# Kernel optimization log

Measured on AMD Instinct MI355X. Metric: run time of the kernel, lower is better.

Reference implementation:

```python
import jax, jax.numpy as jnp
import numpy as np

DIM = 1024


def setup_inputs() -> dict:
    key = jax.random.key(0)
    kx, kq, kk, kv, kp = jax.random.split(key, 5)
    scale = 1.0 / np.sqrt(DIM)  # ~PyTorch Linear init scale
    return {
        "x": jax.random.normal(kx, (4, 4096, DIM), dtype=jnp.float32),
        "Wq": jax.random.normal(kq, (DIM, DIM), dtype=jnp.float32) * scale,
        "Wk": jax.random.normal(kk, (DIM, DIM), dtype=jnp.float32) * scale,
        "Wv": jax.random.normal(kv, (DIM, DIM), dtype=jnp.float32) * scale,
        "Wp": jax.random.normal(kp, (DIM, DIM), dtype=jnp.float32) * scale,
    }


def reference(x, Wq, Wk, Wv, Wp):
    # nn.Linear: y = x @ W^T (no bias)
    q = jnp.einsum("bsd,ed->bse", x, Wq)
    k = jnp.einsum("bsd,ed->bse", x, Wk)
    v = jnp.einsum("bsd,ed->bse", x, Wv)
    dim = x.shape[-1]
    # maxP 'readout' scaling: 1/dim (instead of 1/sqrt(dim))
    scores = jnp.einsum("bqd,bkd->bqk", q, k) / dim
    attn = jax.nn.softmax(scores, axis=-1)
    out = jnp.einsum("bqk,bkd->bqd", attn, v)
    return jnp.einsum("bsd,ed->bse", out, Wp)
```

## Files before the change

### kernel.cpp

```cpp
#include <hip/hip_runtime.h>

typedef unsigned short u16;
typedef __attribute__((ext_vector_type(8))) short bf16x8;
typedef __attribute__((ext_vector_type(4))) float f32x4;
typedef __attribute__((ext_vector_type(4))) unsigned short us4;
typedef __attribute__((ext_vector_type(8))) unsigned short us8;

__device__ __forceinline__ u16 f2us(float f) {
  union { float f; unsigned u; } a; a.f = f;
  unsigned u = a.u;
  u += 0x7fffu + ((u >> 16) & 1u);
  return (u16)(u >> 16);
}
__device__ __forceinline__ float us2f(u16 h) {
  union { unsigned u; float f; } a; a.u = ((unsigned)h) << 16;
  return a.f;
}

#define GLDS(g, l) __builtin_amdgcn_global_load_lds( \
    (const __attribute__((address_space(1))) void*)(g), \
    (__attribute__((address_space(3))) void*)(l), 16, 0, 0)

__global__ __launch_bounds__(256) void convert_all(
    const float* __restrict__ x, const float* __restrict__ Wq,
    const float* __restrict__ Wk, const float* __restrict__ Wv,
    const float* __restrict__ Wp, u16* __restrict__ xb, u16* __restrict__ wb) {
  const int bid = blockIdx.x;
  const float* src;
  u16* dst;
  int off;
  if (bid < 16384) {
    src = x; dst = xb; off = bid * 256 + threadIdx.x;
  } else {
    const int w = (bid - 16384) >> 10;
    const int lb = (bid - 16384) & 1023;
    src = (w == 0) ? Wq : (w == 1) ? Wk : (w == 2) ? Wv : Wp;
    dst = wb + (size_t)w * 1048576;
    off = lb * 256 + threadIdx.x;
  }
  f32x4 v = ((const f32x4*)src)[off];
  us4 o;
  o.x = f2us(v.x); o.y = f2us(v.y); o.z = f2us(v.z); o.w = f2us(v.w);
  ((us4*)dst)[off] = o;
}

#define MFMA_QUAD(QR, QC)                                                        \
  do {                                                                           \
    __builtin_amdgcn_s_setprio(1);                                               \
    _Pragma("unroll") for (int m = 0; m < 4; ++m)                                \
    _Pragma("unroll") for (int n = 0; n < 2; ++n)                                \
    _Pragma("unroll") for (int s = 0; s < 2; ++s)                                \
      acc[(QR)*4 + m][(QC)*2 + n] = __builtin_amdgcn_mfma_f32_16x16x32_bf16(     \
          af[(QR)*4 + m][s], bf[(QC)*2 + n][s], acc[(QR)*4 + m][(QC)*2 + n],     \
          0, 0, 0);                                                              \
    __builtin_amdgcn_s_setprio(0);                                               \
  } while (0)

#define STAGE_A(buf, h, kb)                                                  \
  do {                                                                       \
    const int su_ = (h) * 128 * lda + (kb);                                  \
    GLDS(Ap + aoff0 + su_, As + (buf) * 16384 + (h) * 8192 + ldst0);         \
    GLDS(Ap + aoff1 + su_, As + (buf) * 16384 + (h) * 8192 + ldst1);         \
  } while (0)

#define STAGE_B(buf, h, kb)                                                  \
  do {                                                                       \
    const int su_ = (h) * 128 * ldb + (kb);                                  \
    GLDS(Bp + boff0 + su_, Bs + (buf) * 16384 + (h) * 8192 + ldst0);         \
    GLDS(Bp + boff1 + su_, Bs + (buf) * 16384 + (h) * 8192 + ldst1);         \
  } while (0)

template <int EP>
__global__ __launch_bounds__(512, 2) void gemm256(
    const u16* __restrict__ A0, const u16* __restrict__ A1,
    const u16* __restrict__ A2, const u16* __restrict__ A3,
    const u16* __restrict__ B0, const u16* __restrict__ B1,
    const u16* __restrict__ B2, const u16* __restrict__ B3,
    void* C0, void* C1, void* C2, void* C3,
    int K, int lda, int ldb, int ldc, float scale) {
  __shared__ u16 As[32768];
  __shared__ u16 Bs[32768];
  const int tid = threadIdx.x;
  const int lane = tid & 63;
  const int wid = tid >> 6;
  const int wm = wid >> 2;
  const int wn = wid & 3;
  const int z = blockIdx.z;
  const u16* A = (z == 0) ? A0 : (z == 1) ? A1 : (z == 2) ? A2 : A3;
  const u16* B = (z == 0) ? B0 : (z == 1) ? B1 : (z == 2) ? B2 : B3;
  void* C = (z == 0) ? C0 : (z == 1) ? C1 : (z == 2) ? C2 : C3;

  const int gx = gridDim.x;
  const int nwg = gx * (int)gridDim.y;
  const int orig = (int)blockIdx.y * gx + (int)blockIdx.x;
  const int swz = (orig & 7) * (nwg >> 3) + (orig >> 3);
  const long trow = (long)(swz / gx) * 256;
  const long tcol = (long)(swz % gx) * 256;

  const int srow = tid >> 3;
  const int sgrp = (tid & 7) ^ (srow & 7);
  const int aoff0 = srow * lda + sgrp * 8;
  const int aoff1 = aoff0 + (lda << 6);
  const int boff0 = srow * ldb + sgrp * 8;
  const int boff1 = boff0 + (ldb << 6);
  const int ldst0 = (tid & ~63) * 8;
  const int ldst1 = ldst0 + 4096;
  const u16* Ap = A + trow * lda;
  const u16* Bp = B + tcol * ldb;

  const int l15x64 = (lane & 15) * 64;
  const int cs0 = ((((lane >> 4) * 8)) ^ ((lane & 7) * 8)) + l15x64;
  const int cs1 = ((32 + ((lane >> 4) * 8)) ^ ((lane & 7) * 8)) + l15x64;

  f32x4 acc[8][4];
  f32x4 zero = {0.f, 0.f, 0.f, 0.f};
#pragma unroll
  for (int m = 0; m < 8; ++m)
#pragma unroll
    for (int n = 0; n < 4; ++n) acc[m][n] = zero;

  const int NT = K >> 6;
  const int kmask = K - 1;

  STAGE_A(0, 0, 0);
  STAGE_A(0, 1, 0);
  STAGE_B(0, 0, 0);
  STAGE_B(0, 1, 0);
  STAGE_A(1, 0, 64 & kmask);
  STAGE_A(1, 1, 64 & kmask);
  asm volatile("s_waitcnt vmcnt(4)" ::: "memory");
  __builtin_amdgcn_s_barrier();

  for (int t = 0; t < NT; ++t) {
    const int cur = t & 1, nxt = cur ^ 1;
    const int kb1 = ((t + 1) << 6) & kmask;
    const int kb2 = ((t + 2) << 6) & kmask;
    const u16* Acur = As + cur * 16384 + wm * 8192;
    const u16* Bcur = Bs + cur * 16384 + (wn >> 1) * 8192 + (wn & 1) * 4096;
    bf16x8 af[8][2], bf[4][2];

#pragma unroll
    for (int m = 0; m < 4; ++m) {
      af[m][0] = *(const bf16x8*)(Acur + m * 1024 + cs0);
      af[m][1] = *(const bf16x8*)(Acur + m * 1024 + cs1);
    }
#pragma unroll
    for (int n = 0; n < 2; ++n) {
      bf[n][0] = *(const bf16x8*)(Bcur + n * 1024 + cs0);
      bf[n][1] = *(const bf16x8*)(Bcur + n * 1024 + cs1);
    }
    STAGE_B(nxt, 0, kb1);
    __builtin_amdgcn_s_barrier();
    MFMA_QUAD(0, 0);

#pragma unroll
    for (int m = 0; m < 4; ++m) {
      af[4 + m][0] = *(const bf16x8*)(Acur + (4 + m) * 1024 + cs0);
      af[4 + m][1] = *(const bf16x8*)(Acur + (4 + m) * 1024 + cs1);
    }
    STAGE_B(nxt, 1, kb1);
    __builtin_amdgcn_s_barrier();
    MFMA_QUAD(1, 0);

#pragma unroll
    for (int n = 0; n < 2; ++n) {
      bf[2 + n][0] = *(const bf16x8*)(Bcur + (2 + n) * 1024 + cs0);
      bf[2 + n][1] = *(const bf16x8*)(Bcur + (2 + n) * 1024 + cs1);
    }
    __builtin_amdgcn_s_barrier();
    MFMA_QUAD(0, 1);

    STAGE_A(cur, 0, kb2);
    STAGE_A(cur, 1, kb2);
    __builtin_amdgcn_s_barrier();
    MFMA_QUAD(1, 1);
    asm volatile("s_waitcnt vmcnt(4)" ::: "memory");
  }

  asm volatile("s_waitcnt vmcnt(0)" ::: "memory");

  if (EP == 0 || (EP == 3 && z != 2)) {
    u16* Cb = (u16*)C;
#pragma unroll
    for (int m = 0; m < 8; ++m) {
      int gr = (int)trow + wm * 128 + m * 16 + ((lane >> 4) << 2);
#pragma unroll
      for (int n = 0; n < 4; ++n) {
        int gc = (int)tcol + wn * 64 + n * 16 + (lane & 15);
        f32x4 v = acc[m][n];
#pragma unroll
        for (int j = 0; j < 4; ++j) Cb[(size_t)(gr + j) * ldc + gc] = f2us(v[j] * scale);
      }
    }
  } else if (EP == 3) {
    u16* Ct = (u16*)C;
#pragma unroll
    for (int m = 0; m < 8; ++m) {
      int gr = (int)trow + wm * 128 + m * 16 + ((lane >> 4) << 2);
      int b = gr >> 12;
      int sl = gr & 4095;
      u16* base = Ct + ((size_t)b << 22) + sl;
#pragma unroll
      for (int n = 0; n < 4; ++n) {
        int gc = (int)tcol + wn * 64 + n * 16 + (lane & 15);
        f32x4 v = acc[m][n];
        us4 o;
        o.x = f2us(v[0] * scale); o.y = f2us(v[1] * scale);
        o.z = f2us(v[2] * scale); o.w = f2us(v[3] * scale);
        *(us4*)(base + (size_t)gc * 4096) = o;
      }
    }
  } else {
    float* Cf = (float*)C;
#pragma unroll
    for (int m = 0; m < 8; ++m) {
      int gr = (int)trow + wm * 128 + m * 16 + ((lane >> 4) << 2);
#pragma unroll
      for (int n = 0; n < 4; ++n) {
        int gc = (int)tcol + wn * 64 + n * 16 + (lane & 15);
        f32x4 v = acc[m][n];
#pragma unroll
        for (int j = 0; j < 4; ++j) Cf[(size_t)(gr + j) * ldc + gc] = v[j] * scale;
      }
    }
  }
}

__global__ __launch_bounds__(256) void softmax_all(u16* S0, u16* S1, u16* S2, u16* S3) {
  const int row = blockIdx.x;
  const int b = row >> 12;
  u16* S = (b == 0) ? S0 : (b == 1) ? S1 : (b == 2) ? S2 : S3;
  const int t = threadIdx.x;
  const int lane = t & 63;
  const int wave = t >> 6;
  u16* p = S + (size_t)(row & 4095) * 4096 + t * 16;
  us8 r0 = *(const us8*)p;
  us8 r1 = *(const us8*)(p + 8);
  float f[16];
#pragma unroll
  for (int j = 0; j < 8; ++j) { f[j] = us2f(r0[j]); f[8 + j] = us2f(r1[j]); }

  float mx = f[0];
#pragma unroll
  for (int j = 1; j < 16; ++j) mx = fmaxf(mx, f[j]);
#pragma unroll
  for (int o = 32; o > 0; o >>= 1) mx = fmaxf(mx, __shfl_xor(mx, o));
  __shared__ float rmax[4], rsum[4];
  if (lane == 0) rmax[wave] = mx;
  __syncthreads();
  mx = fmaxf(fmaxf(rmax[0], rmax[1]), fmaxf(rmax[2], rmax[3]));

  float e[16], s = 0.f;
#pragma unroll
  for (int j = 0; j < 16; ++j) { e[j] = __expf(f[j] - mx); s += e[j]; }
#pragma unroll
  for (int o = 32; o > 0; o >>= 1) s += __shfl_xor(s, o);
  if (lane == 0) rsum[wave] = s;
  __syncthreads();
  s = rsum[0] + rsum[1] + rsum[2] + rsum[3];
  float inv = 1.f / s;

  us8 o0, o1;
#pragma unroll
  for (int j = 0; j < 8; ++j) { o0[j] = f2us(e[j] * inv); o1[j] = f2us(e[8 + j] * inv); }
  *(us8*)p = o0;
  *(us8*)(p + 8) = o1;
}

extern "C" void kernel_launch(void* const* d_in, const int* in_sizes, int n_in,
                              void* d_out, int out_size, void* d_ws, size_t ws_size,
                              hipStream_t stream) {
  (void)in_sizes; (void)n_in; (void)out_size;
  const float* x  = (const float*)d_in[0];
  const float* Wq = (const float*)d_in[1];
  const float* Wk = (const float*)d_in[2];
  const float* Wv = (const float*)d_in[3];
  const float* Wp = (const float*)d_in[4];

  if (ws_size < 209715200) return;
  char* ws = (char*)d_ws;
  u16* xb  = (u16*)(ws);
  u16* wqb = (u16*)(ws + 33554432);
  u16* wkb = wqb + 1048576;
  u16* wvb = wkb + 1048576;
  u16* wpb = wvb + 1048576;
  u16* Qb  = (u16*)(ws + 41943040);
  u16* Kb  = (u16*)(ws + 75497472);
  u16* Vt  = (u16*)(ws + 109051904);
  u16* Ssp = (u16*)(ws + 142606336);
  u16* O   = (u16*)(ws + 176160768);

  u16* S0 = (u16*)d_out;
  u16* S1 = S0 + 16777216;
  u16* S2 = xb;
  u16* S3 = Ssp;

  convert_all<<<20480, 256, 0, stream>>>(x, Wq, Wk, Wv, Wp, xb, wqb);

  gemm256<3><<<dim3(4, 64, 3), 512, 0, stream>>>(
      xb, xb, xb, xb, wqb, wkb, wvb, wvb, Qb, Kb, Vt, Vt,
      1024, 1024, 1024, 1024, 1.f);

  const u16 *Q0 = Qb, *Q1 = Qb + 4194304, *Q2 = Qb + 8388608, *Q3 = Qb + 12582912;
  const u16 *K0 = Kb, *K1 = Kb + 4194304, *K2 = Kb + 8388608, *K3 = Kb + 12582912;
  gemm256<0><<<dim3(16, 16, 4), 512, 0, stream>>>(Q0, Q1, Q2, Q3, K0, K1, K2, K3,
                                                  S0, S1, S2, S3, 1024, 1024, 1024, 4096,
                                                  1.f / 1024.f);

  softmax_all<<<16384, 256, 0, stream>>>(S0, S1, S2, S3);

  const u16 *V0 = Vt, *V1 = Vt + 4194304, *V2 = Vt + 8388608, *V3 = Vt + 12582912;
  u16 *O0 = O, *O1 = O + 4194304, *O2 = O + 8388608, *O3 = O + 12582912;
  gemm256<0><<<dim3(4, 16, 4), 512, 0, stream>>>(S0, S1, S2, S3, V0, V1, V2, V3,
                                                 O0, O1, O2, O3, 4096, 4096, 4096, 1024, 1.f);

  gemm256<2><<<dim3(4, 64, 1), 512, 0, stream>>>(O, O, O, O, wpb, wpb, wpb, wpb,
                                                 d_out, d_out, d_out, d_out,
                                                 1024, 1024, 1024, 1024, 1.f);
}
```

Baseline: 438.0 us.

## Switch GEMM inner loop from 16x16x32 to 32x32x16 bf16 MFMA tiles

Replaces the 16x16x32 MFMA fragments with 32x32x16 MFMA instructions. This changes the per-wave accumulator layout to 4x2 tiles of 32x32, the LDS fragment addressing (swizzled offsets over 32 rows and four k-slices), and all three epilogues so they match the new output lane mapping. Larger MFMA tiles cut the number of LDS fragment reads and MFMA issues per FLOP. The costs are longer-latency instructions, different register pressure, and epilogue stores that are less contiguous in some paths.

```diff
diff --git a/kernel.cpp b/kernel.cpp
--- a/kernel.cpp
+++ b/kernel.cpp
@@ -3,6 +3,7 @@
 typedef unsigned short u16;
 typedef __attribute__((ext_vector_type(8))) short bf16x8;
 typedef __attribute__((ext_vector_type(4))) float f32x4;
+typedef __attribute__((ext_vector_type(16))) float f32x16;
 typedef __attribute__((ext_vector_type(4))) unsigned short us4;
 typedef __attribute__((ext_vector_type(8))) unsigned short us8;
 
@@ -44,15 +45,15 @@
   ((us4*)dst)[off] = o;
 }
 
-#define MFMA_QUAD(QR, QC)                                                        \
+#define MFMA_PAIR(MA, MB, NT)                                                    \
   do {                                                                           \
     __builtin_amdgcn_s_setprio(1);                                               \
-    _Pragma("unroll") for (int m = 0; m < 4; ++m)                                \
-    _Pragma("unroll") for (int n = 0; n < 2; ++n)                                \
-    _Pragma("unroll") for (int s = 0; s < 2; ++s)                                \
-      acc[(QR)*4 + m][(QC)*2 + n] = __builtin_amdgcn_mfma_f32_16x16x32_bf16(     \
-          af[(QR)*4 + m][s], bf[(QC)*2 + n][s], acc[(QR)*4 + m][(QC)*2 + n],     \
-          0, 0, 0);                                                              \
+    _Pragma("unroll") for (int ks = 0; ks < 4; ++ks) {                           \
+      acc[MA][NT] = __builtin_amdgcn_mfma_f32_32x32x16_bf16(                     \
+          af[MA][ks], bf[NT][ks], acc[MA][NT], 0, 0, 0);                         \
+      acc[MB][NT] = __builtin_amdgcn_mfma_f32_32x32x16_bf16(                     \
+          af[MB][ks], bf[NT][ks], acc[MB][NT], 0, 0, 0);                         \
+    }                                                                            \
     __builtin_amdgcn_s_setprio(0);                                               \
   } while (0)
 
@@ -108,16 +109,19 @@
   const u16* Ap = A + trow * lda;
   const u16* Bp = B + tcol * ldb;
 
-  const int l15x64 = (lane & 15) * 64;
-  const int cs0 = ((((lane >> 4) * 8)) ^ ((lane & 7) * 8)) + l15x64;
-  const int cs1 = ((32 + ((lane >> 4) * 8)) ^ ((lane & 7) * 8)) + l15x64;
-
-  f32x4 acc[8][4];
-  f32x4 zero = {0.f, 0.f, 0.f, 0.f};
-#pragma unroll
-  for (int m = 0; m < 8; ++m)
-#pragma unroll
-    for (int n = 0; n < 4; ++n) acc[m][n] = zero;
+  const int l31x64 = (lane & 31) * 64;
+  const int cb = (lane >> 5) * 8;
+  const int xr = (lane & 7) * 8;
+  const int cs_[4] = {((0 + cb) ^ xr) + l31x64, ((16 + cb) ^ xr) + l31x64,
+                      ((32 + cb) ^ xr) + l31x64, ((48 + cb) ^ xr) + l31x64};
+
+  f32x16 acc[4][2];
+#pragma unroll
+  for (int mt = 0; mt < 4; ++mt)
+#pragma unroll
+    for (int nt = 0; nt < 2; ++nt)
+#pragma unroll
+      for (int j = 0; j < 16; ++j) acc[mt][nt][j] = 0.f;
 
   const int NT = K >> 6;
   const int kmask = K - 1;
@@ -137,43 +141,37 @@
     const int kb2 = ((t + 2) << 6) & kmask;
     const u16* Acur = As + cur * 16384 + wm * 8192;
     const u16* Bcur = Bs + cur * 16384 + (wn >> 1) * 8192 + (wn & 1) * 4096;
-    bf16x8 af[8][2], bf[4][2];
-
-#pragma unroll
-    for (int m = 0; m < 4; ++m) {
-      af[m][0] = *(const bf16x8*)(Acur + m * 1024 + cs0);
-      af[m][1] = *(const bf16x8*)(Acur + m * 1024 + cs1);
-    }
-#pragma unroll
-    for (int n = 0; n < 2; ++n) {
-      bf[n][0] = *(const bf16x8*)(Bcur + n * 1024 + cs0);
-      bf[n][1] = *(const bf16x8*)(Bcur + n * 1024 + cs1);
+    bf16x8 af[4][4], bf[2][4];
+
+#pragma unroll
+    for (int ks = 0; ks < 4; ++ks) {
+      af[0][ks] = *(const bf16x8*)(Acur + 0 * 2048 + cs_[ks]);
+      af[1][ks] = *(const bf16x8*)(Acur + 1 * 2048 + cs_[ks]);
+      bf[0][ks] = *(const bf16x8*)(Bcur + 0 * 2048 + cs_[ks]);
     }
     STAGE_B(nxt, 0, kb1);
     __builtin_amdgcn_s_barrier();
-    MFMA_QUAD(0, 0);
-
-#pragma unroll
-    for (int m = 0; m < 4; ++m) {
-      af[4 + m][0] = *(const bf16x8*)(Acur + (4 + m) * 1024 + cs0);
-      af[4 + m][1] = *(const bf16x8*)(Acur + (4 + m) * 1024 + cs1);
+    MFMA_PAIR(0, 1, 0);
+
+#pragma unroll
+    for (int ks = 0; ks < 4; ++ks) {
+      af[2][ks] = *(const bf16x8*)(Acur + 2 * 2048 + cs_[ks]);
+      af[3][ks] = *(const bf16x8*)(Acur + 3 * 2048 + cs_[ks]);
     }
     STAGE_B(nxt, 1, kb1);
     __builtin_amdgcn_s_barrier();
-    MFMA_QUAD(1, 0);
-
-#pragma unroll
-    for (int n = 0; n < 2; ++n) {
-      bf[2 + n][0] = *(const bf16x8*)(Bcur + (2 + n) * 1024 + cs0);
-      bf[2 + n][1] = *(const bf16x8*)(Bcur + (2 + n) * 1024 + cs1);
-    }
+    MFMA_PAIR(2, 3, 0);
+
+#pragma unroll
+    for (int ks = 0; ks < 4; ++ks)
+      bf[1][ks] = *(const bf16x8*)(Bcur + 1 * 2048 + cs_[ks]);
     __builtin_amdgcn_s_barrier();
-    MFMA_QUAD(0, 1);
+    MFMA_PAIR(0, 1, 1);
 
     STAGE_A(cur, 0, kb2);
     STAGE_A(cur, 1, kb2);
     __builtin_amdgcn_s_barrier();
-    MFMA_QUAD(1, 1);
+    MFMA_PAIR(2, 3, 1);
     asm volatile("s_waitcnt vmcnt(4)" ::: "memory");
   }
 
@@ -182,47 +180,53 @@
   if (EP == 0 || (EP == 3 && z != 2)) {
     u16* Cb = (u16*)C;
 #pragma unroll
-    for (int m = 0; m < 8; ++m) {
-      int gr = (int)trow + wm * 128 + m * 16 + ((lane >> 4) << 2);
-#pragma unroll
-      for (int n = 0; n < 4; ++n) {
-        int gc = (int)tcol + wn * 64 + n * 16 + (lane & 15);
-        f32x4 v = acc[m][n];
-#pragma unroll
-        for (int j = 0; j < 4; ++j) Cb[(size_t)(gr + j) * ldc + gc] = f2us(v[j] * scale);
+    for (int mt = 0; mt < 4; ++mt)
+#pragma unroll
+      for (int nt = 0; nt < 2; ++nt) {
+        const int gc = (int)tcol + wn * 64 + nt * 32 + (lane & 31);
+        const int gr0 = (int)trow + wm * 128 + mt * 32 + ((lane >> 5) << 2);
+        f32x16 v = acc[mt][nt];
+#pragma unroll
+        for (int j = 0; j < 16; ++j) {
+          const int row = gr0 + (j & 3) + ((j >> 2) << 3);
+          Cb[(size_t)row * ldc + gc] = f2us(v[j] * scale);
+        }
       }
-    }
   } else if (EP == 3) {
     u16* Ct = (u16*)C;
 #pragma unroll
-    for (int m = 0; m < 8; ++m) {
-      int gr = (int)trow + wm * 128 + m * 16 + ((lane >> 4) << 2);
-      int b = gr >> 12;
-      int sl = gr & 4095;
-      u16* base = Ct + ((size_t)b << 22) + sl;
-#pragma unroll
-      for (int n = 0; n < 4; ++n) {
-        int gc = (int)tcol + wn * 64 + n * 16 + (lane & 15);
-        f32x4 v = acc[m][n];
-        us4 o;
-        o.x = f2us(v[0] * scale); o.y = f2us(v[1] * scale);
-        o.z = f2us(v[2] * scale); o.w = f2us(v[3] * scale);
-        *(us4*)(base + (size_t)gc * 4096) = o;
+    for (int mt = 0; mt < 4; ++mt)
+#pragma unroll
+      for (int nt = 0; nt < 2; ++nt) {
+        const int gc = (int)tcol + wn * 64 + nt * 32 + (lane & 31);
+        const int gr0 = (int)trow + wm * 128 + mt * 32 + ((lane >> 5) << 2);
+        f32x16 v = acc[mt][nt];
+#pragma unroll
+        for (int g = 0; g < 4; ++g) {
+          const int s = gr0 + (g << 3);
+          const int b = s >> 12;
+          const int sl = s & 4095;
+          us4 o;
+          o.x = f2us(v[4 * g + 0] * scale); o.y = f2us(v[4 * g + 1] * scale);
+          o.z = f2us(v[4 * g + 2] * scale); o.w = f2us(v[4 * g + 3] * scale);
+          *(us4*)(Ct + ((size_t)b << 22) + (size_t)gc * 4096 + sl) = o;
+        }
       }
-    }
   } else {
     float* Cf = (float*)C;
 #pragma unroll
-    for (int m = 0; m < 8; ++m) {
-      int gr = (int)trow + wm * 128 + m * 16 + ((lane >> 4) << 2);
-#pragma unroll
-      for (int n = 0; n < 4; ++n) {
-        int gc = (int)tcol + wn * 64 + n * 16 + (lane & 15);
-        f32x4 v = acc[m][n];
-#pragma unroll
-        for (int j = 0; j < 4; ++j) Cf[(size_t)(gr + j) * ldc + gc] = v[j] * scale;
+    for (int mt = 0; mt < 4; ++mt)
+#pragma unroll
+      for (int nt = 0; nt < 2; ++nt) {
+        const int gc = (int)tcol + wn * 64 + nt * 32 + (lane & 31);
+        const int gr0 = (int)trow + wm * 128 + mt * 32 + ((lane >> 5) << 2);
+        f32x16 v = acc[mt][nt];
+#pragma unroll
+        for (int j = 0; j < 16; ++j) {
+          const int row = gr0 + (j & 3) + ((j >> 2) << 3);
+          Cf[(size_t)row * ldc + gc] = v[j] * scale;
+        }
       }
-    }
   }
 }
 
```

After: 483.3 us. 10.4% more time.

## Fuse exp into QK^T epilogue and defer softmax normalization to PV epilogue

Applied to the files above, without the earlier changes.

The QK^T GEMM epilogue now writes exp(score/dim) directly, without subtracting the row max. A light kernel computes only the reciprocal row sums into a float buffer reused from the Q region. The PV GEMM epilogue then scales each output row by that reciprocal. This removes the softmax kernel's rewrite of the full score matrix and its max reduction. Skipping the max subtraction relies on scores staying small enough, given the 1/dim scaling, that exp does not overflow.

```diff
diff --git a/kernel.cpp b/kernel.cpp
--- a/kernel.cpp
+++ b/kernel.cpp
@@ -77,7 +77,8 @@
     const u16* __restrict__ B0, const u16* __restrict__ B1,
     const u16* __restrict__ B2, const u16* __restrict__ B3,
     void* C0, void* C1, void* C2, void* C3,
-    int K, int lda, int ldb, int ldc, float scale) {
+    int K, int lda, int ldb, int ldc, float scale,
+    const float* __restrict__ rsinv) {
   __shared__ u16 As[32768];
   __shared__ u16 Bs[32768];
   const int tid = threadIdx.x;
@@ -210,6 +211,35 @@
         *(us4*)(base + (size_t)gc * 4096) = o;
       }
     }
+  } else if (EP == 4) {
+    u16* Cb = (u16*)C;
+#pragma unroll
+    for (int m = 0; m < 8; ++m) {
+      int gr = (int)trow + wm * 128 + m * 16 + ((lane >> 4) << 2);
+#pragma unroll
+      for (int n = 0; n < 4; ++n) {
+        int gc = (int)tcol + wn * 64 + n * 16 + (lane & 15);
+        f32x4 v = acc[m][n];
+#pragma unroll
+        for (int j = 0; j < 4; ++j)
+          Cb[(size_t)(gr + j) * ldc + gc] = f2us(__expf(v[j] * scale));
+      }
+    }
+  } else if (EP == 5) {
+    const float* rs = rsinv + z * 4096;
+    u16* Cb = (u16*)C;
+#pragma unroll
+    for (int m = 0; m < 8; ++m) {
+      int gr = (int)trow + wm * 128 + m * 16 + ((lane >> 4) << 2);
+      f32x4 rv = *(const f32x4*)&rs[gr];
+#pragma unroll
+      for (int n = 0; n < 4; ++n) {
+        int gc = (int)tcol + wn * 64 + n * 16 + (lane & 15);
+        f32x4 v = acc[m][n];
+#pragma unroll
+        for (int j = 0; j < 4; ++j) Cb[(size_t)(gr + j) * ldc + gc] = f2us(v[j] * rv[j]);
+      }
+    }
   } else {
     float* Cf = (float*)C;
 #pragma unroll
@@ -226,45 +256,28 @@
   }
 }
 
-__global__ __launch_bounds__(256) void softmax_all(u16* S0, u16* S1, u16* S2, u16* S3) {
+__global__ __launch_bounds__(256) void rowsum_inv(
+    const u16* __restrict__ S0, const u16* __restrict__ S1,
+    const u16* __restrict__ S2, const u16* __restrict__ S3,
+    float* __restrict__ rsinv) {
   const int row = blockIdx.x;
   const int b = row >> 12;
-  u16* S = (b == 0) ? S0 : (b == 1) ? S1 : (b == 2) ? S2 : S3;
+  const u16* S = (b == 0) ? S0 : (b == 1) ? S1 : (b == 2) ? S2 : S3;
   const int t = threadIdx.x;
   const int lane = t & 63;
   const int wave = t >> 6;
-  u16* p = S + (size_t)(row & 4095) * 4096 + t * 16;
+  const u16* p = S + (size_t)(row & 4095) * 4096 + t * 16;
   us8 r0 = *(const us8*)p;
   us8 r1 = *(const us8*)(p + 8);
-  float f[16];
-#pragma unroll
-  for (int j = 0; j < 8; ++j) { f[j] = us2f(r0[j]); f[8 + j] = us2f(r1[j]); }
-
-  float mx = f[0];
-#pragma unroll
-  for (int j = 1; j < 16; ++j) mx = fmaxf(mx, f[j]);
-#pragma unroll
-  for (int o = 32; o > 0; o >>= 1) mx = fmaxf(mx, __shfl_xor(mx, o));
-  __shared__ float rmax[4], rsum[4];
-  if (lane == 0) rmax[wave] = mx;
-  __syncthreads();
-  mx = fmaxf(fmaxf(rmax[0], rmax[1]), fmaxf(rmax[2], rmax[3]));
-
-  float e[16], s = 0.f;
-#pragma unroll
-  for (int j = 0; j < 16; ++j) { e[j] = __expf(f[j] - mx); s += e[j]; }
+  float s = 0.f;
+#pragma unroll
+  for (int j = 0; j < 8; ++j) s += us2f(r0[j]) + us2f(r1[j]);
 #pragma unroll
   for (int o = 32; o > 0; o >>= 1) s += __shfl_xor(s, o);
+  __shared__ float rsum[4];
   if (lane == 0) rsum[wave] = s;
   __syncthreads();
-  s = rsum[0] + rsum[1] + rsum[2] + rsum[3];
-  float inv = 1.f / s;
-
-  us8 o0, o1;
-#pragma unroll
-  for (int j = 0; j < 8; ++j) { o0[j] = f2us(e[j] * inv); o1[j] = f2us(e[8 + j] * inv); }
-  *(us8*)p = o0;
-  *(us8*)(p + 8) = o1;
+  if (t == 0) rsinv[row] = 1.f / (rsum[0] + rsum[1] + rsum[2] + rsum[3]);
 }
 
 extern "C" void kernel_launch(void* const* d_in, const int* in_sizes, int n_in,
@@ -294,27 +307,29 @@
   u16* S1 = S0 + 16777216;
   u16* S2 = xb;
   u16* S3 = Ssp;
+  float* rsinv = (float*)Qb;
 
   convert_all<<<20480, 256, 0, stream>>>(x, Wq, Wk, Wv, Wp, xb, wqb);
 
   gemm256<3><<<dim3(4, 64, 3), 512, 0, stream>>>(
       xb, xb, xb, xb, wqb, wkb, wvb, wvb, Qb, Kb, Vt, Vt,
-      1024, 1024, 1024, 1024, 1.f);
+      1024, 1024, 1024, 1024, 1.f, nullptr);
 
   const u16 *Q0 = Qb, *Q1 = Qb + 4194304, *Q2 = Qb + 8388608, *Q3 = Qb + 12582912;
   const u16 *K0 = Kb, *K1 = Kb + 4194304, *K2 = Kb + 8388608, *K3 = Kb + 12582912;
-  gemm256<0><<<dim3(16, 16, 4), 512, 0, stream>>>(Q0, Q1, Q2, Q3, K0, K1, K2, K3,
+  gemm256<4><<<dim3(16, 16, 4), 512, 0, stream>>>(Q0, Q1, Q2, Q3, K0, K1, K2, K3,
                                                   S0, S1, S2, S3, 1024, 1024, 1024, 4096,
-                                                  1.f / 1024.f);
-
-  softmax_all<<<16384, 256, 0, stream>>>(S0, S1, S2, S3);
+                                                  1.f / 1024.f, nullptr);
+
+  rowsum_inv<<<16384, 256, 0, stream>>>(S0, S1, S2, S3, rsinv);
 
   const u16 *V0 = Vt, *V1 = Vt + 4194304, *V2 = Vt + 8388608, *V3 = Vt + 12582912;
   u16 *O0 = O, *O1 = O + 4194304, *O2 = O + 8388608, *O3 = O + 12582912;
-  gemm256<0><<<dim3(4, 16, 4), 512, 0, stream>>>(S0, S1, S2, S3, V0, V1, V2, V3,
-                                                 O0, O1, O2, O3, 4096, 4096, 4096, 1024, 1.f);
+  gemm256<5><<<dim3(4, 16, 4), 512, 0, stream>>>(S0, S1, S2, S3, V0, V1, V2, V3,
+                                                 O0, O1, O2, O3, 4096, 4096, 4096, 1024,
+                                                 1.f, rsinv);
 
   gemm256<2><<<dim3(4, 64, 1), 512, 0, stream>>>(O, O, O, O, wpb, wpb, wpb, wpb,
                                                  d_out, d_out, d_out, d_out,
-                                                 1024, 1024, 1024, 1024, 1.f);
-}
+                                                 1024, 1024, 1024, 1024, 1.f, nullptr);
+}
```

After: 427.0 us. 1.03x faster.
